# Optimization experiments

Hardware: AMD Instinct MI355X
Metric: run time of the kernel (lower is better)

Reference implementation:

```python
import jax, jax.numpy as jnp
import numpy as np

BASE_TEMP = 0.07
CLASS_TEMPS = jnp.array([0.08, 0.05, 0.10], dtype=jnp.float32)  # idx 0,1,2
EPS = 1e-08


def setup_inputs() -> dict:
    key = jax.random.key(0)
    k1, k2 = jax.random.split(key)
    B, D = 8192, 128
    embeddings = jax.random.normal(k1, (B, D), dtype=jnp.float32)
    labels = jax.random.randint(k2, (B,), 0, 3, dtype=jnp.int64)
    return {"embeddings": embeddings, "labels": labels}


def reference(embeddings, labels):
    B = embeddings.shape[0]
    # per-row temperature from the row's class label
    temps = CLASS_TEMPS[labels]  # [B]
    sim = jnp.matmul(embeddings, embeddings.T)  # [B, B]
    logits = sim / temps[:, None]
    # subtract detached row max (stability, gradient-stopped as in .detach())
    logits = logits - jax.lax.stop_gradient(jnp.max(logits, axis=1, keepdims=True))
    # denominator includes the self term (original sums exp over all j)
    log_prob = logits - jnp.log(jnp.sum(jnp.exp(logits), axis=1, keepdims=True) + EPS)
    # positives: same label, excluding self
    pos_mask = (labels[:, None] == labels[None, :]).astype(jnp.float32)
    pos_mask = pos_mask * (1.0 - jnp.eye(B, dtype=jnp.float32))
    pos_count = jnp.sum(pos_mask, axis=1)  # [B]
    valid = pos_count > 0
    loss_i = -(BASE_TEMP / temps) * jnp.sum(pos_mask * log_prob, axis=1) / (pos_count + EPS)
    n_valid = jnp.sum(valid.astype(jnp.float32))
    total = jnp.sum(jnp.where(valid, loss_i, 0.0))
    return jnp.where(n_valid > 0, total / jnp.maximum(n_valid, 1.0), 0.0)
```

## Files before the change

kernel.cpp:

```cpp
#include <hip/hip_runtime.h>
#include <hip/hip_bf16.h>


#define B_ROWS 8192
#define D_DIM 128
#define BASE_TEMP 0.07f
#define LOG2E 1.4426950408889634f
#define LN2 0.6931471805599453f

typedef __bf16 bf16x8 __attribute__((ext_vector_type(8)));
typedef __bf16 bf16x4 __attribute__((ext_vector_type(4)));
typedef float floatx16 __attribute__((ext_vector_type(16)));

__device__ __forceinline__ float class_invtemp(int lbl) {
    return (lbl == 0) ? 12.5f : ((lbl == 1) ? 20.0f : 10.0f);
}

__global__ __launch_bounds__(256) void k0_cast_sums(
        const float* __restrict__ E, const int* __restrict__ labels,
        __bf16* __restrict__ Ebf, float* __restrict__ csum ,
        float* __restrict__ ccnt ) {
    const int blk = blockIdx.x;
    const int tid = threadIdx.x;
    const int row0 = blk * 128;

    __shared__ int scnt[3];
    if (tid < 3) scnt[tid] = 0;

    const float4* src = reinterpret_cast<const float4*>(E + (size_t)row0 * D_DIM);
    #pragma unroll
    for (int p = 0; p < 16; ++p) {
        int idx = p * 256 + tid;
        float4 v = src[idx];
        int r = idx >> 5, k4 = idx & 31;
        int R = row0 + r;
        int T = R >> 5;
        int l = (R & 31) + ((k4 >> 1) & 1) * 32;
        int c = k4 >> 2;
        size_t dst = (size_t)T * 4096 + c * 512 + l * 8 + (k4 & 1) * 4;
        bf16x4 o = { (__bf16)v.x, (__bf16)v.y, (__bf16)v.z, (__bf16)v.w };
        *reinterpret_cast<bf16x4*>(Ebf + dst) = o;
    }

    const int d = tid & 127, half = tid >> 7;
    float s0 = 0.f, s1 = 0.f, s2 = 0.f;
    #pragma unroll 4
    for (int r2 = 0; r2 < 64; ++r2) {
        int r = row0 + half * 64 + r2;
        float v = E[(size_t)r * D_DIM + d];
        int l = labels[r];
        s0 += (l == 0) ? v : 0.f;
        s1 += (l == 1) ? v : 0.f;
        s2 += (l == 2) ? v : 0.f;
    }
    __shared__ float sh[3][128];
    if (half == 1) { sh[0][d] = s0; sh[1][d] = s1; sh[2][d] = s2; }
    __syncthreads();
    if (half == 0) {
        csum[((size_t)blk * 3 + 0) * 128 + d] = s0 + sh[0][d];
        csum[((size_t)blk * 3 + 1) * 128 + d] = s1 + sh[1][d];
        csum[((size_t)blk * 3 + 2) * 128 + d] = s2 + sh[2][d];
    }
    if (tid < 128) atomicAdd(&scnt[labels[row0 + tid]], 1);
    __syncthreads();
    if (tid < 3) ccnt[blk * 4 + tid] = (float)scnt[tid];
}

__global__ __launch_bounds__(256) void k0b_reduce(
        const float* __restrict__ csum, const float* __restrict__ ccnt,
        float* __restrict__ S , float* __restrict__ counts ) {
    const int tid = threadIdx.x;
    if (tid < 128) {
        #pragma unroll
        for (int c = 0; c < 3; ++c) {
            float a = 0.f;
            #pragma unroll 8
            for (int blk = 0; blk < 64; ++blk)
                a += csum[((size_t)blk * 3 + c) * 128 + tid];
            S[c * 128 + tid] = a;
        }
    } else if (tid < 131) {
        int c = tid - 128;
        float a = 0.f;
        #pragma unroll 8
        for (int blk = 0; blk < 64; ++blk) a += ccnt[blk * 4 + c];
        counts[c] = a;
    }
}

__global__ __launch_bounds__(256, 3) void k2_stats(
        const __bf16* __restrict__ Ebf, const int* __restrict__ labels,
        float2* __restrict__ part, int nsplit, int jrange) {
    const int lane = threadIdx.x & 63;
    const int wave = threadIdx.x >> 6;
    const int split = blockIdx.y;
    const int j0 = split * jrange;
    const int col = lane & 31;
    const int icol = blockIdx.x * 128 + wave * 32 + col;

    const float bscale = class_invtemp(labels[icol]) * LOG2E;

    const int iT = blockIdx.x * 4 + wave;
    const __bf16* bbase = Ebf + (size_t)iT * 4096 + lane * 8;
    bf16x8 Bf[8];
    #pragma unroll
    for (int c = 0; c < 8; ++c) {
        bf16x8 raw = *reinterpret_cast<const bf16x8*>(bbase + c * 512);
        bf16x8 sc;
        #pragma unroll
        for (int e = 0; e < 8; ++e) sc[e] = (__bf16)((float)raw[e] * bscale);
        Bf[c] = sc;
    }

    const __bf16* abase = Ebf + ((size_t)(j0 >> 5)) * 4096 + lane * 8;
    bf16x8 A0[8], A1[8];
    #pragma unroll
    for (int c = 0; c < 8; ++c)
        A0[c] = *reinterpret_cast<const bf16x8*>(abase + c * 512);

    float m[2] = { -3.0e38f, -3.0e38f };
    float Z[2] = { 0.f, 0.f };
    const int nsteps = jrange >> 5;

    auto k2_step = [&](const bf16x8* Ab, int ch) {
        floatx16 a0, a1;
        #pragma unroll
        for (int r = 0; r < 16; ++r) { a0[r] = 0.f; a1[r] = 0.f; }
        a0 = __builtin_amdgcn_mfma_f32_32x32x16_bf16(Ab[0], Bf[0], a0, 0, 0, 0);
        a1 = __builtin_amdgcn_mfma_f32_32x32x16_bf16(Ab[4], Bf[4], a1, 0, 0, 0);
        a0 = __builtin_amdgcn_mfma_f32_32x32x16_bf16(Ab[1], Bf[1], a0, 0, 0, 0);
        a1 = __builtin_amdgcn_mfma_f32_32x32x16_bf16(Ab[5], Bf[5], a1, 0, 0, 0);
        a0 = __builtin_amdgcn_mfma_f32_32x32x16_bf16(Ab[2], Bf[2], a0, 0, 0, 0);
        a1 = __builtin_amdgcn_mfma_f32_32x32x16_bf16(Ab[6], Bf[6], a1, 0, 0, 0);
        a0 = __builtin_amdgcn_mfma_f32_32x32x16_bf16(Ab[3], Bf[3], a0, 0, 0, 0);
        a1 = __builtin_amdgcn_mfma_f32_32x32x16_bf16(Ab[7], Bf[7], a1, 0, 0, 0);
        float v[16];
        #pragma unroll
        for (int r = 0; r < 16; ++r) v[r] = a0[r] + a1[r];
        float x0 = fmaxf(v[0], v[1]),   x1 = fmaxf(v[2], v[3]);
        float x2 = fmaxf(v[4], v[5]),   x3 = fmaxf(v[6], v[7]);
        float x4 = fmaxf(v[8], v[9]),   x5 = fmaxf(v[10], v[11]);
        float x6 = fmaxf(v[12], v[13]), x7 = fmaxf(v[14], v[15]);
        float mx = fmaxf(fmaxf(fmaxf(x0, x1), fmaxf(x2, x3)),
                         fmaxf(fmaxf(x4, x5), fmaxf(x6, x7)));
        float nm = fmaxf(m[ch], mx);
        float z[16];
        #pragma unroll
        for (int r = 0; r < 16; ++r) z[r] = __builtin_amdgcn_exp2f(v[r] - nm);
        float t0 = (z[0] + z[1]) + (z[2] + z[3]);
        float t1 = (z[4] + z[5]) + (z[6] + z[7]);
        float t2 = (z[8] + z[9]) + (z[10] + z[11]);
        float t3 = (z[12] + z[13]) + (z[14] + z[15]);
        Z[ch] = fmaf(Z[ch], __builtin_amdgcn_exp2f(m[ch] - nm), (t0 + t1) + (t2 + t3));
        m[ch] = nm;
    };

    for (int s = 0; s < nsteps; s += 2) {
        {
            const __bf16* ap = abase + (size_t)(s + 1) * 4096;
            #pragma unroll
            for (int c = 0; c < 8; ++c)
                A1[c] = *reinterpret_cast<const bf16x8*>(ap + c * 512);
            k2_step(A0, 0);
        }
        {
            if (s + 2 < nsteps) {
                const __bf16* ap = abase + (size_t)(s + 2) * 4096;
                #pragma unroll
                for (int c = 0; c < 8; ++c)
                    A0[c] = *reinterpret_cast<const bf16x8*>(ap + c * 512);
            }
            k2_step(A1, 1);
        }
    }

    float nm = fmaxf(m[0], m[1]);
    float Zm = Z[0] * __builtin_amdgcn_exp2f(m[0] - nm)
             + Z[1] * __builtin_amdgcn_exp2f(m[1] - nm);

    float om = __shfl_xor(nm, 32), oZ = __shfl_xor(Zm, 32);
    float fm = fmaxf(nm, om);
    float fZ = Zm * __builtin_amdgcn_exp2f(nm - fm)
             + oZ * __builtin_amdgcn_exp2f(om - fm);
    if (lane < 32)
        part[(size_t)icol * nsplit + split] = make_float2(fm, fZ);
}

__global__ __launch_bounds__(256) void k3_rowloss(
        const float* __restrict__ E, const int* __restrict__ labels,
        const float* __restrict__ S, const float* __restrict__ counts,
        const float2* __restrict__ part, int nsplit,
        float* __restrict__ bpart ) {
    __shared__ float sS[3][128];
    const int tid = threadIdx.x;
    if (tid < 128) {
        sS[0][tid] = S[tid];
        sS[1][tid] = S[128 + tid];
        sS[2][tid] = S[256 + tid];
    }
    __syncthreads();

    const int i = blockIdx.x * 256 + tid;
    const int lab = labels[i];
    const float invt = class_invtemp(lab);

    const float4* er = reinterpret_cast<const float4*>(E + (size_t)i * D_DIM);
    const float4* sr = reinterpret_cast<const float4*>(&sS[lab][0]);
    float dotS = 0.f, nrm = 0.f;
    #pragma unroll
    for (int k4 = 0; k4 < 32; ++k4) {
        float4 v = er[k4];
        float4 s = sr[k4];
        dotS += v.x * s.x + v.y * s.y + v.z * s.z + v.w * s.w;
        nrm  += v.x * v.x + v.y * v.y + v.z * v.z + v.w * v.w;
    }

    float m = -3.0e38f, Z = 0.f;
    for (int sp = 0; sp < nsplit; ++sp) {
        float2 p = part[(size_t)i * nsplit + sp];
        float nm = fmaxf(m, p.x);
        Z = Z * __builtin_amdgcn_exp2f(m - nm) + p.y * __builtin_amdgcn_exp2f(p.x - nm);
        m = nm;
    }

    const float C = counts[lab] - 1.0f;
    const float M_nat = m * LN2;
    const float lnZ = LN2 * __builtin_amdgcn_logf(Z + 1e-8f);
    const float P_nat = invt * (dotS - nrm);
    float loss = -(BASE_TEMP * invt) * (P_nat - C * (M_nat + lnZ)) / (C + 1e-8f);
    float valid = (C > 0.f) ? 1.f : 0.f;
    loss = (C > 0.f) ? loss : 0.f;

    #pragma unroll
    for (int off = 32; off; off >>= 1) {
        loss += __shfl_down(loss, off);
        valid += __shfl_down(valid, off);
    }
    __shared__ float rs[4][2];
    const int w = tid >> 6;
    if ((tid & 63) == 0) { rs[w][0] = loss; rs[w][1] = valid; }
    __syncthreads();
    if (tid == 0) {
        bpart[blockIdx.x * 2 + 0] = rs[0][0] + rs[1][0] + rs[2][0] + rs[3][0];
        bpart[blockIdx.x * 2 + 1] = rs[0][1] + rs[1][1] + rs[2][1] + rs[3][1];
    }
}

__global__ void k4_final(const float* __restrict__ bpart, float* __restrict__ out) {
    const int lane = threadIdx.x;
    float T = 0.f, N = 0.f;
    if (lane < 32) { T = bpart[lane * 2]; N = bpart[lane * 2 + 1]; }
    #pragma unroll
    for (int off = 32; off; off >>= 1) {
        T += __shfl_down(T, off);
        N += __shfl_down(N, off);
    }
    if (lane == 0) out[0] = (N > 0.f) ? T / fmaxf(N, 1.f) : 0.f;
}

extern "C" void kernel_launch(void* const* d_in, const int* in_sizes, int n_in,
                              void* d_out, int out_size, void* d_ws, size_t ws_size,
                              hipStream_t stream) {
    const float* E = (const float*)d_in[0];
    const int* labels = (const int*)d_in[1];
    float* out = (float*)d_out;
    char* ws = (char*)d_ws;

    const size_t OFF_EBF = 0;
    const size_t OFF_CSUM = (size_t)2 << 20;
    const size_t OFF_CCNT = OFF_CSUM + 98304;
    const size_t OFF_S = OFF_CCNT + 1024;
    const size_t OFF_CNT = OFF_S + 1536;
    const size_t OFF_BPART = OFF_CNT + 64;
    const size_t OFF_PART = OFF_CSUM + (128 << 10);

    int nsplit = 4;
    if (ws_size >= OFF_PART + (size_t)B_ROWS * 16 * 8) nsplit = 16;
    else if (ws_size >= OFF_PART + (size_t)B_ROWS * 8 * 8) nsplit = 8;
    const int jrange = B_ROWS / nsplit;

    __bf16* Ebf = (__bf16*)(ws + OFF_EBF);
    float* csum = (float*)(ws + OFF_CSUM);
    float* ccnt = (float*)(ws + OFF_CCNT);
    float* S = (float*)(ws + OFF_S);
    float* counts = (float*)(ws + OFF_CNT);
    float* bpart = (float*)(ws + OFF_BPART);
    float2* part = (float2*)(ws + OFF_PART);

    k0_cast_sums<<<64, 256, 0, stream>>>(E, labels, Ebf, csum, ccnt);
    k0b_reduce<<<1, 256, 0, stream>>>(csum, ccnt, S, counts);
    k2_stats<<<dim3(64, nsplit), 256, 0, stream>>>(Ebf, labels, part, nsplit, jrange);
    k3_rowloss<<<32, 256, 0, stream>>>(E, labels, S, counts, part, nsplit, bpart);
    k4_final<<<1, 64, 0, stream>>>(bpart, out);
}
```

Measured before the change: 54.42 us.

## Use self-similarity as fixed row max and replace reductions with fixed-point atomics

The online softmax running max is replaced by a known bound: the row's self-similarity (scaled norm), computed in the prep kernel and preloaded into the MFMA accumulator. This lets the exp loop drop its per-step max reduction and rescaling. Cross-block sums of class vectors, counts and losses now go through deterministic 64-bit fixed-point atomics, which removes the separate reduce kernel, and the split count rises. It depends on Cauchy-Schwarz holding under bf16 rounding, which may let exp exceed 1 slightly, and it adds a memset launch.

```diff
diff --git a/kernel.cpp b/kernel.cpp
--- a/kernel.cpp
+++ b/kernel.cpp
@@ -7,6 +7,7 @@
 #define BASE_TEMP 0.07f
 #define LOG2E 1.4426950408889634f
 #define LN2 0.6931471805599453f
+#define FIX_SCALE 1048576.0f
 
 typedef __bf16 bf16x8 __attribute__((ext_vector_type(8)));
 typedef __bf16 bf16x4 __attribute__((ext_vector_type(4)));
@@ -16,20 +17,26 @@
     return (lbl == 0) ? 12.5f : ((lbl == 1) ? 20.0f : 10.0f);
 }
 
-__global__ __launch_bounds__(256) void k0_cast_sums(
+__device__ __forceinline__ unsigned long long fix64(float v) {
+    return (unsigned long long)(long long)llrintf(v * FIX_SCALE);
+}
+
+__global__ __launch_bounds__(256) void k0_prep(
         const float* __restrict__ E, const int* __restrict__ labels,
-        __bf16* __restrict__ Ebf, float* __restrict__ csum ,
-        float* __restrict__ ccnt ) {
+        __bf16* __restrict__ Ebf, float* __restrict__ nrm,
+        unsigned long long* __restrict__ Sfix ,
+        unsigned long long* __restrict__ cntfix ) {
     const int blk = blockIdx.x;
     const int tid = threadIdx.x;
-    const int row0 = blk * 128;
-
+    const int row0 = blk * 32;
+
+    __shared__ float sh[3][128];
     __shared__ int scnt[3];
     if (tid < 3) scnt[tid] = 0;
 
     const float4* src = reinterpret_cast<const float4*>(E + (size_t)row0 * D_DIM);
     #pragma unroll
-    for (int p = 0; p < 16; ++p) {
+    for (int p = 0; p < 4; ++p) {
         int idx = p * 256 + tid;
         float4 v = src[idx];
         int r = idx >> 5, k4 = idx & 31;
@@ -42,55 +49,47 @@
         *reinterpret_cast<bf16x4*>(Ebf + dst) = o;
     }
 
+    {
+        int r = tid >> 3, g = tid & 7;
+        const float4* er = reinterpret_cast<const float4*>(
+            E + (size_t)(row0 + r) * D_DIM + g * 16);
+        float s = 0.f;
+        #pragma unroll
+        for (int q = 0; q < 4; ++q) {
+            float4 v = er[q];
+            s += v.x * v.x + v.y * v.y + v.z * v.z + v.w * v.w;
+        }
+        s += __shfl_xor(s, 1); s += __shfl_xor(s, 2); s += __shfl_xor(s, 4);
+        if (g == 0) nrm[row0 + r] = s;
+    }
+
     const int d = tid & 127, half = tid >> 7;
     float s0 = 0.f, s1 = 0.f, s2 = 0.f;
     #pragma unroll 4
-    for (int r2 = 0; r2 < 64; ++r2) {
-        int r = row0 + half * 64 + r2;
+    for (int r2 = 0; r2 < 16; ++r2) {
+        int r = row0 + half * 16 + r2;
         float v = E[(size_t)r * D_DIM + d];
         int l = labels[r];
         s0 += (l == 0) ? v : 0.f;
         s1 += (l == 1) ? v : 0.f;
         s2 += (l == 2) ? v : 0.f;
     }
-    __shared__ float sh[3][128];
     if (half == 1) { sh[0][d] = s0; sh[1][d] = s1; sh[2][d] = s2; }
     __syncthreads();
     if (half == 0) {
-        csum[((size_t)blk * 3 + 0) * 128 + d] = s0 + sh[0][d];
-        csum[((size_t)blk * 3 + 1) * 128 + d] = s1 + sh[1][d];
-        csum[((size_t)blk * 3 + 2) * 128 + d] = s2 + sh[2][d];
-    }
-    if (tid < 128) atomicAdd(&scnt[labels[row0 + tid]], 1);
-    __syncthreads();
-    if (tid < 3) ccnt[blk * 4 + tid] = (float)scnt[tid];
-}
-
-__global__ __launch_bounds__(256) void k0b_reduce(
-        const float* __restrict__ csum, const float* __restrict__ ccnt,
-        float* __restrict__ S , float* __restrict__ counts ) {
-    const int tid = threadIdx.x;
-    if (tid < 128) {
-        #pragma unroll
-        for (int c = 0; c < 3; ++c) {
-            float a = 0.f;
-            #pragma unroll 8
-            for (int blk = 0; blk < 64; ++blk)
-                a += csum[((size_t)blk * 3 + c) * 128 + tid];
-            S[c * 128 + tid] = a;
-        }
-    } else if (tid < 131) {
-        int c = tid - 128;
-        float a = 0.f;
-        #pragma unroll 8
-        for (int blk = 0; blk < 64; ++blk) a += ccnt[blk * 4 + c];
-        counts[c] = a;
-    }
+        atomicAdd(&Sfix[d],       fix64(s0 + sh[0][d]));
+        atomicAdd(&Sfix[128 + d], fix64(s1 + sh[1][d]));
+        atomicAdd(&Sfix[256 + d], fix64(s2 + sh[2][d]));
+    }
+    if (tid < 32) atomicAdd(&scnt[labels[row0 + tid]], 1);
+    __syncthreads();
+    if (tid < 3) atomicAdd(&cntfix[tid], (unsigned long long)scnt[tid]);
 }
 
 __global__ __launch_bounds__(256, 3) void k2_stats(
         const __bf16* __restrict__ Ebf, const int* __restrict__ labels,
-        float2* __restrict__ part, int nsplit, int jrange) {
+        const float* __restrict__ nrm, float* __restrict__ part,
+        int nsplit, int jrange) {
     const int lane = threadIdx.x & 63;
     const int wave = threadIdx.x >> 6;
     const int split = blockIdx.y;
@@ -99,6 +98,7 @@
     const int icol = blockIdx.x * 128 + wave * 32 + col;
 
     const float bscale = class_invtemp(labels[icol]) * LOG2E;
+    const float m = bscale * nrm[icol];
 
     const int iT = blockIdx.x * 4 + wave;
     const __bf16* bbase = Ebf + (size_t)iT * 4096 + lane * 8;
@@ -118,14 +118,13 @@
     for (int c = 0; c < 8; ++c)
         A0[c] = *reinterpret_cast<const bf16x8*>(abase + c * 512);
 
-    float m[2] = { -3.0e38f, -3.0e38f };
-    float Z[2] = { 0.f, 0.f };
+    float Z0 = 0.f, Z1 = 0.f;
     const int nsteps = jrange >> 5;
 
-    auto k2_step = [&](const bf16x8* Ab, int ch) {
+    auto k2_step = [&](const bf16x8* Ab, float& Zc) {
         floatx16 a0, a1;
         #pragma unroll
-        for (int r = 0; r < 16; ++r) { a0[r] = 0.f; a1[r] = 0.f; }
+        for (int r = 0; r < 16; ++r) { a0[r] = -m; a1[r] = 0.f; }
         a0 = __builtin_amdgcn_mfma_f32_32x32x16_bf16(Ab[0], Bf[0], a0, 0, 0, 0);
         a1 = __builtin_amdgcn_mfma_f32_32x32x16_bf16(Ab[4], Bf[4], a1, 0, 0, 0);
         a0 = __builtin_amdgcn_mfma_f32_32x32x16_bf16(Ab[1], Bf[1], a0, 0, 0, 0);
@@ -134,25 +133,15 @@
         a1 = __builtin_amdgcn_mfma_f32_32x32x16_bf16(Ab[6], Bf[6], a1, 0, 0, 0);
         a0 = __builtin_amdgcn_mfma_f32_32x32x16_bf16(Ab[3], Bf[3], a0, 0, 0, 0);
         a1 = __builtin_amdgcn_mfma_f32_32x32x16_bf16(Ab[7], Bf[7], a1, 0, 0, 0);
-        float v[16];
-        #pragma unroll
-        for (int r = 0; r < 16; ++r) v[r] = a0[r] + a1[r];
-        float x0 = fmaxf(v[0], v[1]),   x1 = fmaxf(v[2], v[3]);
-        float x2 = fmaxf(v[4], v[5]),   x3 = fmaxf(v[6], v[7]);
-        float x4 = fmaxf(v[8], v[9]),   x5 = fmaxf(v[10], v[11]);
-        float x6 = fmaxf(v[12], v[13]), x7 = fmaxf(v[14], v[15]);
-        float mx = fmaxf(fmaxf(fmaxf(x0, x1), fmaxf(x2, x3)),
-                         fmaxf(fmaxf(x4, x5), fmaxf(x6, x7)));
-        float nm = fmaxf(m[ch], mx);
         float z[16];
         #pragma unroll
-        for (int r = 0; r < 16; ++r) z[r] = __builtin_amdgcn_exp2f(v[r] - nm);
+        for (int r = 0; r < 16; ++r)
+            z[r] = __builtin_amdgcn_exp2f(a0[r] + a1[r]);
         float t0 = (z[0] + z[1]) + (z[2] + z[3]);
         float t1 = (z[4] + z[5]) + (z[6] + z[7]);
         float t2 = (z[8] + z[9]) + (z[10] + z[11]);
         float t3 = (z[12] + z[13]) + (z[14] + z[15]);
-        Z[ch] = fmaf(Z[ch], __builtin_amdgcn_exp2f(m[ch] - nm), (t0 + t1) + (t2 + t3));
-        m[ch] = nm;
+        Zc += (t0 + t1) + (t2 + t3);
     };
 
     for (int s = 0; s < nsteps; s += 2) {
@@ -161,7 +150,7 @@
             #pragma unroll
             for (int c = 0; c < 8; ++c)
                 A1[c] = *reinterpret_cast<const bf16x8*>(ap + c * 512);
-            k2_step(A0, 0);
+            k2_step(A0, Z0);
         }
         {
             if (s + 2 < nsteps) {
@@ -170,65 +159,54 @@
                 for (int c = 0; c < 8; ++c)
                     A0[c] = *reinterpret_cast<const bf16x8*>(ap + c * 512);
             }
-            k2_step(A1, 1);
+            k2_step(A1, Z1);
         }
     }
 
-    float nm = fmaxf(m[0], m[1]);
-    float Zm = Z[0] * __builtin_amdgcn_exp2f(m[0] - nm)
-             + Z[1] * __builtin_amdgcn_exp2f(m[1] - nm);
-
-    float om = __shfl_xor(nm, 32), oZ = __shfl_xor(Zm, 32);
-    float fm = fmaxf(nm, om);
-    float fZ = Zm * __builtin_amdgcn_exp2f(nm - fm)
-             + oZ * __builtin_amdgcn_exp2f(om - fm);
+    float Zt = Z0 + Z1;
+    Zt += __shfl_xor(Zt, 32);
     if (lane < 32)
-        part[(size_t)icol * nsplit + split] = make_float2(fm, fZ);
-}
-
-__global__ __launch_bounds__(256) void k3_rowloss(
+        part[(size_t)split * B_ROWS + icol] = Zt;
+}
+
+__global__ __launch_bounds__(128) void k3_rowloss(
         const float* __restrict__ E, const int* __restrict__ labels,
-        const float* __restrict__ S, const float* __restrict__ counts,
-        const float2* __restrict__ part, int nsplit,
-        float* __restrict__ bpart ) {
+        const unsigned long long* __restrict__ Sfix,
+        const unsigned long long* __restrict__ cntfix,
+        const float* __restrict__ nrm, const float* __restrict__ part,
+        int nsplit, unsigned long long* __restrict__ lossfix,
+        unsigned long long* __restrict__ validfix) {
     __shared__ float sS[3][128];
     const int tid = threadIdx.x;
-    if (tid < 128) {
-        sS[0][tid] = S[tid];
-        sS[1][tid] = S[128 + tid];
-        sS[2][tid] = S[256 + tid];
-    }
-    __syncthreads();
-
-    const int i = blockIdx.x * 256 + tid;
+    #pragma unroll
+    for (int c = 0; c < 3; ++c)
+        sS[c][tid] = (float)(long long)Sfix[c * 128 + tid] * (1.0f / FIX_SCALE);
+    __syncthreads();
+
+    const int i = blockIdx.x * 128 + tid;
     const int lab = labels[i];
     const float invt = class_invtemp(lab);
 
     const float4* er = reinterpret_cast<const float4*>(E + (size_t)i * D_DIM);
     const float4* sr = reinterpret_cast<const float4*>(&sS[lab][0]);
-    float dotS = 0.f, nrm = 0.f;
+    float dotS = 0.f;
     #pragma unroll
     for (int k4 = 0; k4 < 32; ++k4) {
         float4 v = er[k4];
         float4 s = sr[k4];
         dotS += v.x * s.x + v.y * s.y + v.z * s.z + v.w * s.w;
-        nrm  += v.x * v.x + v.y * v.y + v.z * v.z + v.w * v.w;
-    }
-
-    float m = -3.0e38f, Z = 0.f;
-    for (int sp = 0; sp < nsplit; ++sp) {
-        float2 p = part[(size_t)i * nsplit + sp];
-        float nm = fmaxf(m, p.x);
-        Z = Z * __builtin_amdgcn_exp2f(m - nm) + p.y * __builtin_amdgcn_exp2f(p.x - nm);
-        m = nm;
-    }
-
-    const float C = counts[lab] - 1.0f;
-    const float M_nat = m * LN2;
-    const float lnZ = LN2 * __builtin_amdgcn_logf(Z + 1e-8f);
-    const float P_nat = invt * (dotS - nrm);
-    float loss = -(BASE_TEMP * invt) * (P_nat - C * (M_nat + lnZ)) / (C + 1e-8f);
-    float valid = (C > 0.f) ? 1.f : 0.f;
+    }
+    const float nr = nrm[i];
+
+    float Zt = 0.f;
+    for (int sp = 0; sp < nsplit; ++sp)
+        Zt += part[(size_t)sp * B_ROWS + i];
+
+    const float C = (float)(long long)cntfix[lab] - 1.0f;
+    const float lse = invt * nr + LN2 * __builtin_amdgcn_logf(Zt);
+    const float P_nat = invt * (dotS - nr);
+    float loss = -(BASE_TEMP * invt) * (P_nat - C * lse) / (C + 1e-8f);
+    int valid = (C > 0.f) ? 1 : 0;
     loss = (C > 0.f) ? loss : 0.f;
 
     #pragma unroll
@@ -236,26 +214,24 @@
         loss += __shfl_down(loss, off);
         valid += __shfl_down(valid, off);
     }
-    __shared__ float rs[4][2];
-    const int w = tid >> 6;
-    if ((tid & 63) == 0) { rs[w][0] = loss; rs[w][1] = valid; }
+    __shared__ float rl[2];
+    __shared__ int rv[2];
+    if ((tid & 63) == 0) { rl[tid >> 6] = loss; rv[tid >> 6] = valid; }
     __syncthreads();
     if (tid == 0) {
-        bpart[blockIdx.x * 2 + 0] = rs[0][0] + rs[1][0] + rs[2][0] + rs[3][0];
-        bpart[blockIdx.x * 2 + 1] = rs[0][1] + rs[1][1] + rs[2][1] + rs[3][1];
-    }
-}
-
-__global__ void k4_final(const float* __restrict__ bpart, float* __restrict__ out) {
-    const int lane = threadIdx.x;
-    float T = 0.f, N = 0.f;
-    if (lane < 32) { T = bpart[lane * 2]; N = bpart[lane * 2 + 1]; }
-    #pragma unroll
-    for (int off = 32; off; off >>= 1) {
-        T += __shfl_down(T, off);
-        N += __shfl_down(N, off);
-    }
-    if (lane == 0) out[0] = (N > 0.f) ? T / fmaxf(N, 1.f) : 0.f;
+        atomicAdd(lossfix, fix64(rl[0] + rl[1]));
+        atomicAdd(validfix, (unsigned long long)(rv[0] + rv[1]));
+    }
+}
+
+__global__ void k4_final(const unsigned long long* __restrict__ lossfix,
+                         const unsigned long long* __restrict__ validfix,
+                         float* __restrict__ out) {
+    if (threadIdx.x == 0) {
+        double T = (double)(long long)lossfix[0] * (1.0 / (double)FIX_SCALE);
+        float N = (float)(long long)validfix[0];
+        out[0] = (N > 0.f) ? (float)(T / (double)fmaxf(N, 1.f)) : 0.f;
+    }
 }
 
 extern "C" void kernel_launch(void* const* d_in, const int* in_sizes, int n_in,
@@ -267,29 +243,27 @@
     char* ws = (char*)d_ws;
 
     const size_t OFF_EBF = 0;
-    const size_t OFF_CSUM = (size_t)2 << 20;
-    const size_t OFF_CCNT = OFF_CSUM + 98304;
-    const size_t OFF_S = OFF_CCNT + 1024;
-    const size_t OFF_CNT = OFF_S + 1536;
-    const size_t OFF_BPART = OFF_CNT + 64;
-    const size_t OFF_PART = OFF_CSUM + (128 << 10);
-
-    int nsplit = 4;
-    if (ws_size >= OFF_PART + (size_t)B_ROWS * 16 * 8) nsplit = 16;
-    else if (ws_size >= OFF_PART + (size_t)B_ROWS * 8 * 8) nsplit = 8;
+    const size_t OFF_ATOM = (size_t)2 << 20;
+    const size_t OFF_NRM = OFF_ATOM + 4096;
+    const size_t OFF_PART = OFF_NRM + (size_t)B_ROWS * 4;
+
+    int nsplit = 8;
+    if (ws_size >= OFF_PART + (size_t)32 * B_ROWS * 4) nsplit = 32;
+    else if (ws_size >= OFF_PART + (size_t)16 * B_ROWS * 4) nsplit = 16;
     const int jrange = B_ROWS / nsplit;
 
     __bf16* Ebf = (__bf16*)(ws + OFF_EBF);
-    float* csum = (float*)(ws + OFF_CSUM);
-    float* ccnt = (float*)(ws + OFF_CCNT);
-    float* S = (float*)(ws + OFF_S);
-    float* counts = (float*)(ws + OFF_CNT);
-    float* bpart = (float*)(ws + OFF_BPART);
-    float2* part = (float2*)(ws + OFF_PART);
-
-    k0_cast_sums<<<64, 256, 0, stream>>>(E, labels, Ebf, csum, ccnt);
-    k0b_reduce<<<1, 256, 0, stream>>>(csum, ccnt, S, counts);
-    k2_stats<<<dim3(64, nsplit), 256, 0, stream>>>(Ebf, labels, part, nsplit, jrange);
-    k3_rowloss<<<32, 256, 0, stream>>>(E, labels, S, counts, part, nsplit, bpart);
-    k4_final<<<1, 64, 0, stream>>>(bpart, out);
-}
+    unsigned long long* Sfix = (unsigned long long*)(ws + OFF_ATOM);
+    unsigned long long* cntfix = Sfix + 384;
+    unsigned long long* lossfix = Sfix + 388;
+    unsigned long long* validfix = Sfix + 389;
+    float* nrm = (float*)(ws + OFF_NRM);
+    float* part = (float*)(ws + OFF_PART);
+
+    hipMemsetAsync(ws + OFF_ATOM, 0, 4096, stream);
+    k0_prep<<<256, 256, 0, stream>>>(E, labels, Ebf, nrm, Sfix, cntfix);
+    k2_stats<<<dim3(64, nsplit), 256, 0, stream>>>(Ebf, labels, nrm, part, nsplit, jrange);
+    k3_rowloss<<<64, 128, 0, stream>>>(E, labels, Sfix, cntfix, nrm, part,
+                                       nsplit, lossfix, validfix);
+    k4_final<<<1, 64, 0, stream>>>(lossfix, validfix, out);
+}
```

Measured after the change: 50.82 us. -6.6%, faster.
